# Performance work log

Measured on AMD Instinct MI355X. Metric: run time of the kernel, lower is better.

The kernel has to match this reference:

```python
import jax, jax.numpy as jnp
import numpy as np
import math

V, D, H, NL, ML = 30000, 1024, 16, 6, 1024
B, L = 2, 1024
DH = D // H
HID = D // 2  # BoundaryLayer hidden_dim = d_model // 2


def _ln(x, g, b):
    # torch LayerNorm: biased variance, eps=1e-5
    m = x.mean(-1, keepdims=True)
    v = jnp.var(x, axis=-1, keepdims=True)
    return (x - m) * jax.lax.rsqrt(v + 1e-5) * g + b


def setup_inputs() -> dict:
    key = jax.random.key(0)
    ks = iter(jax.random.split(key, 64))
    nrm = lambda shape, std=0.02: jax.random.normal(next(ks), shape, jnp.float32) * std

    def xav(shape):
        # xavier_uniform over last two dims (fan_in, fan_out) per layer
        fan_in, fan_out = shape[-2], shape[-1]
        bound = math.sqrt(6.0 / (fan_in + fan_out))
        return jax.random.uniform(next(ks), shape, jnp.float32, -bound, bound)

    inp = {
        "ids": jax.random.randint(next(ks), (B, L), 0, V),
        "embed": nrm((V, D)),              # tied with head
        "pos_enc": nrm((1, ML, D)),
        # per-layer stacked params
        "rg_w": nrm((NL, D, 4)),
        "rg_b": jnp.zeros((NL, 4)),
        "qkv_w": xav((NL, D, 3 * D)),
        "qkv_b": jnp.zeros((NL, 3 * D)),
        "out_w": xav((NL, D, D)),
        "out_b": jnp.zeros((NL, D)),
        "ph_w": xav((NL, D, H)),
        "ph_b": jnp.zeros((NL, H)),
        "res_scale": jnp.full((NL,), 0.1, jnp.float32),
        "ph_scale": jnp.ones((NL,), jnp.float32),
        "ff1_w": xav((NL, D, 4 * D)),
        "ff1_b": jnp.zeros((NL, 4 * D)),
        "ff2_w": xav((NL, 4 * D, D)),
        "ff2_b": jnp.zeros((NL, D)),
        "n1_g": jnp.ones((NL, D)),
        "n1_b": jnp.zeros((NL, D)),
        "n2_g": jnp.ones((NL, D)),
        "n2_b": jnp.zeros((NL, D)),
        # shared boundary MLP
        "bnd_w1": xav((D, HID)),
        "bnd_b1": jnp.zeros((HID,)),
        "bnd_w2": xav((HID, 1)),
        "bnd_b2": jnp.zeros((1,)),
        "fn_g": jnp.ones((D,)),
        "fn_b": jnp.zeros((D,)),
    }
    return inp


def reference(ids, embed, pos_enc, rg_w, rg_b, qkv_w, qkv_b, out_w, out_b,
              ph_w, ph_b, res_scale, ph_scale, ff1_w, ff1_b, ff2_w, ff2_b,
              n1_g, n1_b, n2_g, n2_b, bnd_w1, bnd_b1, bnd_w2, bnd_b2, fn_g, fn_b):
    b, l = ids.shape
    d = embed.shape[1]
    nl = rg_w.shape[0]
    h = ph_w.shape[-1]
    dh = d // h

    x = embed[ids] * math.sqrt(d) + pos_enc[:, :l, :]
    grammar, shocks = [], []
    for i in range(nl):
        # R-Grammar modulation
        rg = jax.nn.sigmoid(x @ rg_w[i] + rg_b[i])                  # [B,L,4]
        grammar.append(rg)
        xm = x * (1.0 + 0.1 * rg.mean(-1, keepdims=True))
        # resonance attention (pre-norm)
        a_in = _ln(xm, n1_g[i], n1_b[i])
        qkv = (a_in @ qkv_w[i] + qkv_b[i]).reshape(b, l, 3, h, dh)
        qkv = jnp.transpose(qkv, (2, 0, 3, 1, 4))                   # [3,B,H,L,dh]
        q, k, v = qkv[0], qkv[1], qkv[2]
        scores = jnp.einsum('bhld,bhmd->bhlm', q, k) / math.sqrt(dh)
        pv = jnp.tanh(ph_scale[i] * (a_in @ ph_w[i] + ph_b[i]))     # [B,L,H]
        pv = jnp.transpose(pv, (0, 2, 1))                           # [B,H,L]
        phase_diff = (pv[..., :, None] - pv[..., None, :]) ** 2     # [B,H,L,L]
        scores = scores - res_scale[i] * phase_diff
        aw = jax.nn.softmax(scores, axis=-1)
        o = jnp.einsum('bhlm,bhmd->bhld', aw, v)
        o = jnp.transpose(o, (0, 2, 1, 3)).reshape(b, l, d)
        x = xm + (o @ out_w[i] + out_b[i])
        # feed-forward (exact GELU, matching torch default)
        f_in = _ln(x, n2_g[i], n2_b[i])
        ff = jax.nn.gelu(f_in @ ff1_w[i] + ff1_b[i], approximate=False) @ ff2_w[i] + ff2_b[i]
        x = x + ff
        # boundary shock score (shared MLP)
        shock = jax.nn.sigmoid(jnp.tanh(x @ bnd_w1 + bnd_b1) @ bnd_w2 + bnd_b2)  # [B,L,1]
        shocks.append(shock)
    x = _ln(x, fn_g, fn_b)
    logits = x @ embed.T                                            # tied head
    gs = jnp.stack(grammar, 0)   # [NL,B,L,4]
    ss = jnp.stack(shocks, 0)    # [NL,B,L,1]
    return (logits, x, gs.mean(0), ss.mean(0), gs, ss)
```

## Files before the change

kernel.cpp:

```cpp
#include <hip/hip_runtime.h>
#include <math.h>

constexpr int NLAYER = 6;
constexpr int B_ = 2;
constexpr int L_ = 1024;
constexpr int D_ = 1024;
constexpr int H_ = 16;
constexpr int DH_ = 64;
constexpr int V_ = 30000;
constexpr int HID_ = 512;
constexpr int BL_ = B_ * L_;

typedef __bf16 bf16_t;
typedef bf16_t bf16x8 __attribute__((ext_vector_type(8)));
typedef bf16_t bf16x4 __attribute__((ext_vector_type(4)));
typedef float  f32x4  __attribute__((ext_vector_type(4)));

#define GLOAD_LDS16(gp, lp)                                                    \
    __builtin_amdgcn_global_load_lds(                                          \
        (const __attribute__((address_space(1))) void*)(gp),                   \
        (__attribute__((address_space(3))) void*)(lp), 16, 0, 0)

__device__ __forceinline__ float sigmoidf_(float z) { return 1.0f / (1.0f + __expf(-z)); }
__device__ __forceinline__ float tanhf_(float z) {
    float a = fabsf(z);
    float e = __expf(-2.0f * a);
    float r = (1.0f - e) / (1.0f + e);
    return copysignf(r, z);
}
__device__ __forceinline__ float gelu_exact_(float z) {
    return 0.5f * z * (1.0f + erff(z * 0.70710678118654752440f));
}

__device__ __forceinline__ bf16x8 pack8_(const float* __restrict__ src) {
    float4 f0 = *(const float4*)(src);
    float4 f1 = *(const float4*)(src + 4);
    bf16x8 v;
    v[0] = (bf16_t)f0.x; v[1] = (bf16_t)f0.y; v[2] = (bf16_t)f0.z; v[3] = (bf16_t)f0.w;
    v[4] = (bf16_t)f1.x; v[5] = (bf16_t)f1.y; v[6] = (bf16_t)f1.z; v[7] = (bf16_t)f1.w;
    return v;
}

__device__ __forceinline__ float block_sum_(float v, float* red) {
    int tid = threadIdx.x;
    red[tid] = v; __syncthreads();
    #pragma unroll
    for (int s = 128; s > 0; s >>= 1) {
        if (tid < s) red[tid] += red[tid + s];
        __syncthreads();
    }
    float r = red[0];
    __syncthreads();
    return r;
}

__global__ __launch_bounds__(256) void embed_k(
    const int* __restrict__ ids, const float* __restrict__ emb,
    const float* __restrict__ pos, float* __restrict__ x)
{
    int t = blockIdx.x, tid = threadIdx.x;
    int id = ids[t];
    int l = t % L_;
    #pragma unroll
    for (int it = 0; it < 4; ++it) {
        int d = it * 256 + tid;
        x[(size_t)t * D_ + d] = emb[(size_t)id * D_ + d] * 32.0f + pos[(size_t)l * D_ + d];
    }
}

__global__ __launch_bounds__(256) void tcw_k(
    const float* s0, bf16_t* d0, int K0, int N0, int c0,
    const float* s1, bf16_t* d1, int K1, int N1, int c1,
    const float* s2, bf16_t* d2, int K2, int N2, int c2,
    const float* s3, bf16_t* d3, int K3, int N3, int c3)
{
    __shared__ float t32[32][33];
    int bid = blockIdx.x;
    const float* s; bf16_t* d; int K, N, base;
    if (bid < c0)      { s = s0; d = d0; K = K0; N = N0; base = 0; }
    else if (bid < c1) { s = s1; d = d1; K = K1; N = N1; base = c0; }
    else if (bid < c2) { s = s2; d = d2; K = K2; N = N2; base = c1; }
    else               { s = s3; d = d3; K = K3; N = N3; base = c2; }
    int tt = bid - base;
    int KT = K >> 5;
    int kt = tt % KT, nt = tt / KT;
    int tid = threadIdx.x, cx = tid & 31, ry = tid >> 5;
    #pragma unroll
    for (int j = 0; j < 4; ++j)
        t32[ry + 8 * j][cx] = s[(size_t)(kt * 32 + ry + 8 * j) * N + nt * 32 + cx];
    __syncthreads();
    int r = tid >> 3, c4 = (tid & 7) * 4;
    bf16x4 v;
    #pragma unroll
    for (int j = 0; j < 4; ++j) v[j] = (bf16_t)t32[c4 + j][r];
    *(bf16x4*)(d + (size_t)(nt * 32 + r) * K + kt * 32 + c4) = v;
}

__global__ __launch_bounds__(256) void cvtb_k(
    const float* __restrict__ s, bf16_t* __restrict__ d, int n8)
{
    for (int i = blockIdx.x * 256 + threadIdx.x; i < n8; i += gridDim.x * 256)
        *(bf16x8*)(d + (size_t)i * 8) = pack8_(s + (size_t)i * 8);
}

__global__ __launch_bounds__(256) void rg_xm_ln_k(
    const float* __restrict__ x, const float* __restrict__ rgw,
    const float* __restrict__ rgb, const float* __restrict__ g,
    const float* __restrict__ b, const float* __restrict__ phw,
    const float* __restrict__ phb, const float* __restrict__ ps_p,
    float* __restrict__ xm, bf16_t* __restrict__ ainb,
    float* __restrict__ pvb, float* __restrict__ gs_out)
{
    int t = blockIdx.x, tid = threadIdx.x;
    __shared__ float xr[D_];
    __shared__ float red[256];
    __shared__ float rgsh[4];

    #pragma unroll
    for (int it = 0; it < 4; ++it) {
        int d = it * 256 + tid;
        xr[d] = x[(size_t)t * D_ + d];
    }
    __syncthreads();

    float a0 = 0.f, a1 = 0.f, a2 = 0.f, a3 = 0.f;
    #pragma unroll
    for (int it = 0; it < 4; ++it) {
        int d = it * 256 + tid;
        float xv = xr[d];
        float4 w = *(const float4*)(rgw + (size_t)d * 4);
        a0 += xv * w.x; a1 += xv * w.y; a2 += xv * w.z; a3 += xv * w.w;
    }
    float s0 = block_sum_(a0, red);
    float s1 = block_sum_(a1, red);
    float s2 = block_sum_(a2, red);
    float s3 = block_sum_(a3, red);
    if (tid == 0) {
        float r0 = sigmoidf_(s0 + rgb[0]);
        float r1 = sigmoidf_(s1 + rgb[1]);
        float r2 = sigmoidf_(s2 + rgb[2]);
        float r3 = sigmoidf_(s3 + rgb[3]);
        rgsh[0] = r0; rgsh[1] = r1; rgsh[2] = r2; rgsh[3] = r3;
        gs_out[(size_t)t * 4 + 0] = r0;
        gs_out[(size_t)t * 4 + 1] = r1;
        gs_out[(size_t)t * 4 + 2] = r2;
        gs_out[(size_t)t * 4 + 3] = r3;
    }
    __syncthreads();
    float factor = 1.0f + 0.025f * (rgsh[0] + rgsh[1] + rgsh[2] + rgsh[3]);

    float sm = 0.f, sq = 0.f;
    float vals[4];
    #pragma unroll
    for (int it = 0; it < 4; ++it) {
        int d = it * 256 + tid;
        float v = xr[d] * factor;
        vals[it] = v;
        xm[(size_t)t * D_ + d] = v;
        sm += v; sq += v * v;
    }
    float mean = block_sum_(sm, red) * (1.0f / D_);
    float msq  = block_sum_(sq, red) * (1.0f / D_);
    float rstd = rsqrtf(msq - mean * mean + 1e-5f);
    #pragma unroll
    for (int it = 0; it < 4; ++it) {
        int d = it * 256 + tid;
        float a = (vals[it] - mean) * rstd * g[d] + b[d];
        ainb[(size_t)t * D_ + d] = (bf16_t)a;
        xr[d] = a;
    }
    __syncthreads();

    {
        int c = tid & 15, grp = tid >> 4;
        float acc = 0.f;
        int k0 = grp * 64;
        #pragma unroll
        for (int kk = 0; kk < 64; ++kk)
            acc += xr[k0 + kk] * phw[(size_t)(k0 + kk) * H_ + c];
        red[tid] = acc;
        __syncthreads();
        if (tid < 16) {
            float s = 0.f;
            #pragma unroll
            for (int gg = 0; gg < 16; ++gg) s += red[gg * 16 + tid];
            pvb[(size_t)t * H_ + tid] = tanhf_(ps_p[0] * (s + phb[tid]));
        }
    }
}

__global__ __launch_bounds__(256) void ln_k(
    const float* __restrict__ in, const float* __restrict__ g,
    const float* __restrict__ b, float* __restrict__ outp,
    bf16_t* __restrict__ outb)
{
    int t = blockIdx.x, tid = threadIdx.x;
    __shared__ float red[256];
    float s1 = 0.f, s2 = 0.f;
    float vals[4];
    #pragma unroll
    for (int it = 0; it < 4; ++it) {
        int d = it * 256 + tid;
        float v = in[(size_t)t * D_ + d];
        vals[it] = v; s1 += v; s2 += v * v;
    }
    float mean = block_sum_(s1, red) * (1.0f / D_);
    float msq  = block_sum_(s2, red) * (1.0f / D_);
    float rstd = rsqrtf(msq - mean * mean + 1e-5f);
    #pragma unroll
    for (int it = 0; it < 4; ++it) {
        int d = it * 256 + tid;
        float v = (vals[it] - mean) * rstd * g[d] + b[d];
        if (outp) outp[(size_t)t * D_ + d] = v;
        if (outb) outb[(size_t)t * D_ + d] = (bf16_t)v;
    }
}

template<int BN>
__global__ __launch_bounds__(256) void gemm_bf_k(
    const bf16_t* __restrict__ A, const bf16_t* __restrict__ Bm,
    const float* __restrict__ bias, const float* __restrict__ resid,
    float* __restrict__ C, bf16_t* __restrict__ Cb,
    int M, int N, int K, int MT, int GW,
    int act, const float* __restrict__ scale_ptr)
{
    constexpr int BM = 128;
    constexpr int BK = 64;
    constexpr int WN = BN / 32;

    __shared__ alignas(16) bf16_t As[BM][BK];
    __shared__ alignas(16) bf16_t Bs[BN][BK];

    const int tid  = threadIdx.x;
    const int lane = tid & 63;
    const int w    = tid >> 6;

    int per = MT * GW;
    int grp = blockIdx.x / per;
    int r   = blockIdx.x % per;
    int mi  = r % MT;
    int ni  = grp * GW + r / MT;
    const int bm = mi * BM;
    const int bn = ni * BN;

    const int wr = (w & 1) * 64;
    const int wc = (w >> 1) * (BN / 2);
    const int rlo = lane & 15, lhi = lane >> 4;
    const int srow = lane >> 3;
    const int scol = (lane & 7) * 8;

    f32x4 acc[4][WN];
    #pragma unroll
    for (int m = 0; m < 4; ++m)
        #pragma unroll
        for (int n = 0; n < WN; ++n) {
            f32x4 z = {0.f, 0.f, 0.f, 0.f};
            acc[m][n] = z;
        }

    for (int kt = 0; kt < K; kt += BK) {
        __syncthreads();
        #pragma unroll
        for (int i = 0; i < 4; ++i) {
            int is = w * 4 + i;
            const bf16_t* gp = A + (size_t)(bm + is * 8 + srow) * K + kt + scol;
            GLOAD_LDS16(gp, &As[is * 8][0]);
        }
        #pragma unroll
        for (int i = 0; i < BN / 32; ++i) {
            int is = w * (BN / 32) + i;
            int row = bn + is * 8 + srow;
            if (row > N - 1) row = N - 1;
            const bf16_t* gp = Bm + (size_t)row * K + kt + scol;
            GLOAD_LDS16(gp, &Bs[is * 8][0]);
        }
        __syncthreads();

        #pragma unroll
        for (int h2 = 0; h2 < 2; ++h2) {
            int ko = h2 * 32 + lhi * 8;
            bf16x8 af[4], bfr[WN];
            #pragma unroll
            for (int m = 0; m < 4; ++m)
                af[m] = *(const bf16x8*)(&As[wr + m * 16 + rlo][ko]);
            #pragma unroll
            for (int n = 0; n < WN; ++n)
                bfr[n] = *(const bf16x8*)(&Bs[wc + n * 16 + rlo][ko]);
            #pragma unroll
            for (int m = 0; m < 4; ++m)
                #pragma unroll
                for (int n = 0; n < WN; ++n)
                    acc[m][n] = __builtin_amdgcn_mfma_f32_16x16x32_bf16(
                        af[m], bfr[n], acc[m][n], 0, 0, 0);
        }
    }

    float scale = scale_ptr ? scale_ptr[0] : 1.0f;
    #pragma unroll
    for (int m = 0; m < 4; ++m) {
        #pragma unroll
        for (int n = 0; n < WN; ++n) {
            int col = bn + wc + n * 16 + rlo;
            if (col >= N) continue;
            #pragma unroll
            for (int i = 0; i < 4; ++i) {
                int row = bm + wr + m * 16 + lhi * 4 + i;
                float v = acc[m][n][i];
                if (bias) v += bias[col];
                if (act == 1)      v = gelu_exact_(v);
                else if (act == 2) v = tanhf_(scale * v);
                if (resid) v += resid[(size_t)row * N + col];
                if (C)  C[(size_t)row * N + col] = v;
                if (Cb) Cb[(size_t)row * N + col] = (bf16_t)v;
            }
        }
    }
}

__global__ __launch_bounds__(256) void attn_mfma_k(
    const bf16_t* __restrict__ qkv, const float* __restrict__ pv,
    const float* __restrict__ res_scale_p, bf16_t* __restrict__ o)
{
    constexpr int QB = 64;
    constexpr int NB = 64;

    __shared__ alignas(16) bf16_t Ks[NB][DH_];
    __shared__ alignas(16) bf16_t Vt[DH_][NB];
    __shared__ alignas(16) bf16_t Pl[4][16][NB];
    __shared__ float pvq_s[QB];
    __shared__ float pvk_s[NB];

    const int qt = blockIdx.x, h = blockIdx.y, b = blockIdx.z;
    const int tid = threadIdx.x;
    const int lane = tid & 63, w = tid >> 6;
    const int rlo = lane & 15, lhi = lane >> 4, l7 = lane & 7;
    const float rs = res_scale_p[0];

    const size_t rowbase = (size_t)(b * L_ + qt * QB);

    bf16x8 qf[2];
    {
        const bf16_t* qrow = qkv + (rowbase + w * 16 + rlo) * 3072 + h * DH_;
        #pragma unroll
        for (int kk = 0; kk < 2; ++kk)
            qf[kk] = *(const bf16x8*)(qrow + kk * 32 + lhi * 8);
    }
    if (tid < QB) pvq_s[tid] = pv[(rowbase + tid) * H_ + h];
    __syncthreads();
    float pvq_r[4];
    #pragma unroll
    for (int r = 0; r < 4; ++r) pvq_r[r] = pvq_s[w * 16 + lhi * 4 + r];

    float m_r[4], l_r[4];
    f32x4 acc_o[4];
    #pragma unroll
    for (int r = 0; r < 4; ++r) { m_r[r] = -1e30f; l_r[r] = 0.f; }
    #pragma unroll
    for (int n = 0; n < 4; ++n) {
        f32x4 z = {0.f, 0.f, 0.f, 0.f};
        acc_o[n] = z;
    }

    bf16_t* pw = &Pl[w][0][0];

    for (int k0 = 0; k0 < L_; k0 += NB) {
        __syncthreads();
        #pragma unroll
        for (int i = 0; i < 2; ++i) {
            int sid = i * 256 + tid;
            int row = sid >> 3, s = sid & 7;
            bf16x8 v = *(const bf16x8*)(qkv + (size_t)(b * L_ + k0 + row) * 3072
                                        + 1024 + h * DH_ + s * 8);
            *(bf16x8*)(&Ks[row][(s ^ (row & 7)) * 8]) = v;
        }
        {
            int col4 = (tid & 15) * 4;
            int kb   = tid >> 4;
            bf16x4 rv[4];
            #pragma unroll
            for (int j = 0; j < 4; ++j)
                rv[j] = *(const bf16x4*)(qkv + (size_t)(b * L_ + k0 + kb * 4 + j) * 3072
                                         + 2048 + h * DH_ + col4);
            #pragma unroll
            for (int jj = 0; jj < 4; ++jj) {
                int col = col4 + jj;
                bf16x4 v;
                #pragma unroll
                for (int j = 0; j < 4; ++j)
                    v[j] = rv[j][jj];
                *(bf16x4*)(&Vt[col][((kb >> 1) ^ (col & 7)) * 8 + (kb & 1) * 4]) = v;
            }
        }
        if (tid < NB) pvk_s[tid] = pv[(size_t)(b * L_ + k0 + tid) * H_ + h];
        __syncthreads();

        f32x4 sacc[4];
        #pragma unroll
        for (int n = 0; n < 4; ++n) {
            f32x4 z = {0.f, 0.f, 0.f, 0.f};
            sacc[n] = z;
        }
        __builtin_amdgcn_s_setprio(1);
        #pragma unroll
        for (int kk = 0; kk < 2; ++kk) {
            int soff = ((kk * 4 + lhi) ^ l7) * 8;
            bf16x8 kf[4];
            #pragma unroll
            for (int n = 0; n < 4; ++n)
                kf[n] = *(const bf16x8*)(&Ks[n * 16 + rlo][soff]);
            #pragma unroll
            for (int n = 0; n < 4; ++n)
                sacc[n] = __builtin_amdgcn_mfma_f32_16x16x32_bf16(
                    qf[kk], kf[n], sacc[n], 0, 0, 0);
        }
        __builtin_amdgcn_s_setprio(0);

        float sv[4][4];
        float tmax[4] = {-1e30f, -1e30f, -1e30f, -1e30f};
        #pragma unroll
        for (int n = 0; n < 4; ++n) {
            float pvk = pvk_s[n * 16 + rlo];
            #pragma unroll
            for (int r = 0; r < 4; ++r) {
                float dd = pvq_r[r] - pvk;
                float s = sacc[n][r] * 0.125f - rs * dd * dd;
                sv[n][r] = s;
                tmax[r] = fmaxf(tmax[r], s);
            }
        }
        #pragma unroll
        for (int st = 1; st < 16; st <<= 1)
            #pragma unroll
            for (int r = 0; r < 4; ++r)
                tmax[r] = fmaxf(tmax[r], __shfl_xor(tmax[r], st));

        float tsum[4] = {0.f, 0.f, 0.f, 0.f};
        #pragma unroll
        for (int r = 0; r < 4; ++r) {
            float mn = fmaxf(m_r[r], tmax[r]);
            float sc = __expf(m_r[r] - mn);
            m_r[r] = mn;
            l_r[r] *= sc;
            #pragma unroll
            for (int n = 0; n < 4; ++n) acc_o[n][r] *= sc;
        }
        #pragma unroll
        for (int n = 0; n < 4; ++n) {
            int key = n * 16 + rlo;
            #pragma unroll
            for (int r = 0; r < 4; ++r) {
                float p = __expf(sv[n][r] - m_r[r]);
                tsum[r] += p;
                int q = lhi * 4 + r;
                pw[q * NB + (((key >> 3) ^ (q & 7)) * 8 + (key & 7))] = (bf16_t)p;
            }
        }
        #pragma unroll
        for (int st = 1; st < 16; st <<= 1)
            #pragma unroll
            for (int r = 0; r < 4; ++r)
                tsum[r] += __shfl_xor(tsum[r], st);
        #pragma unroll
        for (int r = 0; r < 4; ++r) l_r[r] += tsum[r];

        __builtin_amdgcn_s_setprio(1);
        #pragma unroll
        for (int kk = 0; kk < 2; ++kk) {
            int soff = ((kk * 4 + lhi) ^ l7) * 8;
            bf16x8 pa = *(const bf16x8*)(pw + rlo * NB + (((kk * 4 + lhi) ^ (rlo & 7)) * 8));
            bf16x8 vf[4];
            #pragma unroll
            for (int n = 0; n < 4; ++n)
                vf[n] = *(const bf16x8*)(&Vt[n * 16 + rlo][soff]);
            #pragma unroll
            for (int n = 0; n < 4; ++n)
                acc_o[n] = __builtin_amdgcn_mfma_f32_16x16x32_bf16(
                    pa, vf[n], acc_o[n], 0, 0, 0);
        }
        __builtin_amdgcn_s_setprio(0);
    }

    float inv[4];
    #pragma unroll
    for (int r = 0; r < 4; ++r) inv[r] = 1.0f / l_r[r];
    #pragma unroll
    for (int n = 0; n < 4; ++n)
        #pragma unroll
        for (int r = 0; r < 4; ++r)
            o[(rowbase + w * 16 + lhi * 4 + r) * D_ + h * DH_ + n * 16 + rlo] =
                (bf16_t)(acc_o[n][r] * inv[r]);
}

__global__ __launch_bounds__(256) void bnd2_k(
    const float* __restrict__ hbuf, const float* __restrict__ w2,
    const float* __restrict__ b2, float* __restrict__ ss_out)
{
    int t = blockIdx.x, tid = threadIdx.x;
    __shared__ float red[256];
    float acc = 0.f;
    #pragma unroll
    for (int it = 0; it < 2; ++it) {
        int d = it * 256 + tid;
        acc += hbuf[(size_t)t * HID_ + d] * w2[d];
    }
    float s = block_sum_(acc, red);
    if (tid == 0) ss_out[t] = sigmoidf_(s + b2[0]);
}

__global__ __launch_bounds__(256) void means_k(
    const float* __restrict__ gs, const float* __restrict__ ss,
    float* __restrict__ gsm, float* __restrict__ ssm)
{
    int i = blockIdx.x * 256 + threadIdx.x;
    if (i < BL_ * 4) {
        float s = 0.f;
        #pragma unroll
        for (int l = 0; l < NLAYER; ++l) s += gs[(size_t)l * BL_ * 4 + i];
        gsm[i] = s * (1.0f / NLAYER);
    }
    if (i < BL_) {
        float s = 0.f;
        #pragma unroll
        for (int l = 0; l < NLAYER; ++l) s += ss[(size_t)l * BL_ + i];
        ssm[i] = s * (1.0f / NLAYER);
    }
}

extern "C" void kernel_launch(void* const* d_in, const int* in_sizes, int n_in,
                              void* d_out, int out_size, void* d_ws, size_t ws_size,
                              hipStream_t stream) {
    const int*   ids       = (const int*)  d_in[0];
    const float* embed     = (const float*)d_in[1];
    const float* pos_enc   = (const float*)d_in[2];
    const float* rg_w      = (const float*)d_in[3];
    const float* rg_b      = (const float*)d_in[4];
    const float* qkv_w     = (const float*)d_in[5];
    const float* qkv_b     = (const float*)d_in[6];
    const float* out_w     = (const float*)d_in[7];
    const float* out_b     = (const float*)d_in[8];
    const float* ph_w      = (const float*)d_in[9];
    const float* ph_b      = (const float*)d_in[10];
    const float* res_scale = (const float*)d_in[11];
    const float* ph_scale  = (const float*)d_in[12];
    const float* ff1_w     = (const float*)d_in[13];
    const float* ff1_b     = (const float*)d_in[14];
    const float* ff2_w     = (const float*)d_in[15];
    const float* ff2_b     = (const float*)d_in[16];
    const float* n1_g      = (const float*)d_in[17];
    const float* n1_b      = (const float*)d_in[18];
    const float* n2_g      = (const float*)d_in[19];
    const float* n2_b      = (const float*)d_in[20];
    const float* bnd_w1    = (const float*)d_in[21];
    const float* bnd_b1    = (const float*)d_in[22];
    const float* bnd_w2    = (const float*)d_in[23];
    const float* bnd_b2    = (const float*)d_in[24];
    const float* fn_g      = (const float*)d_in[25];
    const float* fn_b      = (const float*)d_in[26];

    float* out = (float*)d_out;
    float* ws  = (float*)d_ws;

    const size_t M1 = 1024 * 1024;
    float*  x    = ws;
    float*  xm   = ws + 2 * M1;
    float*  bndh = ws + 4 * M1;
    float*  pvb  = ws + 5 * M1;
    bf16_t* ainb = (bf16_t*)(ws + 5 * M1 + M1 / 4);
    bf16_t* aob  = (bf16_t*)(ws + 6 * M1 + M1 / 4);
    bf16_t* xb   = (bf16_t*)(ws + 7 * M1 + M1 / 4);
    bf16_t* qkvb = (bf16_t*)(ws + 8 * M1 + M1 / 4);
    bf16_t* ffhb = (bf16_t*)(ws + 11 * M1 + M1 / 4);
    float*  wT   = ws + 15 * M1 + M1 / 4;
    bf16_t* qkvT = (bf16_t*)(wT);
    bf16_t* outT = (bf16_t*)(wT + 1572864);
    bf16_t* ff1T = (bf16_t*)(wT + 2097152);
    bf16_t* ff2T = (bf16_t*)(wT + 4194304);
    bf16_t* bndT = (bf16_t*)(wT + 6291456);
    bf16_t* embB = qkvb;

    const size_t o_logits = 0;
    const size_t o_x      = (size_t)BL_ * V_;
    const size_t o_gsm    = o_x + (size_t)BL_ * D_;
    const size_t o_ssm    = o_gsm + (size_t)BL_ * 4;
    const size_t o_gs     = o_ssm + (size_t)BL_;
    const size_t o_ss     = o_gs + (size_t)NLAYER * BL_ * 4;

    embed_k<<<BL_, 256, 0, stream>>>(ids, embed, pos_enc, x);

    tcw_k<<<512, 256, 0, stream>>>(
        bnd_w1, bndT, D_, HID_, 512,
        bnd_w1, bndT, D_, HID_, 512,
        bnd_w1, bndT, D_, HID_, 512,
        bnd_w1, bndT, D_, HID_, 512);

    const int MT = BL_ / 128;

    for (int i = 0; i < NLAYER; ++i) {
        tcw_k<<<12288, 256, 0, stream>>>(
            qkv_w + (size_t)i * D_ * 3 * D_,    qkvT, D_,     3 * D_, 3072,
            out_w + (size_t)i * D_ * D_,        outT, D_,     D_,     4096,
            ff1_w + (size_t)i * D_ * 4 * D_,    ff1T, D_,     4 * D_, 8192,
            ff2_w + (size_t)i * 4 * D_ * D_,    ff2T, 4 * D_, D_,     12288);

        rg_xm_ln_k<<<BL_, 256, 0, stream>>>(
            x, rg_w + (size_t)i * D_ * 4, rg_b + (size_t)i * 4,
            n1_g + (size_t)i * D_, n1_b + (size_t)i * D_,
            ph_w + (size_t)i * D_ * H_, ph_b + (size_t)i * H_, ph_scale + i,
            xm, ainb, pvb, out + o_gs + (size_t)i * BL_ * 4);

        gemm_bf_k<128><<<MT * 24, 256, 0, stream>>>(
            ainb, qkvT, qkv_b + (size_t)i * 3 * D_, nullptr,
            nullptr, qkvb, BL_, 3 * D_, D_, MT, 4, 0, nullptr);

        dim3 ga(L_ / 64, H_, B_);
        attn_mfma_k<<<ga, 256, 0, stream>>>(qkvb, pvb, res_scale + i, aob);

        gemm_bf_k<64><<<MT * 16, 256, 0, stream>>>(
            aob, outT, out_b + (size_t)i * D_, xm,
            x, nullptr, BL_, D_, D_, MT, 4, 0, nullptr);

        ln_k<<<BL_, 256, 0, stream>>>(x, n2_g + (size_t)i * D_, n2_b + (size_t)i * D_,
                                      nullptr, ainb);

        gemm_bf_k<128><<<MT * 32, 256, 0, stream>>>(
            ainb, ff1T, ff1_b + (size_t)i * 4 * D_, nullptr,
            nullptr, ffhb, BL_, 4 * D_, D_, MT, 4, 1, nullptr);

        gemm_bf_k<64><<<MT * 16, 256, 0, stream>>>(
            ffhb, ff2T, ff2_b + (size_t)i * D_, x,
            x, xb, BL_, D_, 4 * D_, MT, 4, 0, nullptr);

        gemm_bf_k<64><<<MT * 8, 256, 0, stream>>>(
            xb, bndT, bnd_b1, nullptr,
            bndh, nullptr, BL_, HID_, D_, MT, 4, 2, nullptr);

        bnd2_k<<<BL_, 256, 0, stream>>>(bndh, bnd_w2, bnd_b2, out + o_ss + (size_t)i * BL_);
    }

    ln_k<<<BL_, 256, 0, stream>>>(x, fn_g, fn_b, out + o_x, xb);

    cvtb_k<<<4096, 256, 0, stream>>>(embed, embB, V_ * D_ / 8);

    gemm_bf_k<128><<<MT * 235, 256, 0, stream>>>(
        xb, embB, nullptr, nullptr,
        out + o_logits, nullptr, BL_, V_, D_, MT, 5, 0, nullptr);

    means_k<<<(BL_ * 4 + 255) / 256, 256, 0, stream>>>(
        out + o_gs, out + o_ss, out + o_gsm, out + o_ssm);
}
```

Baseline: 2.587 ms.

## Double-buffer attention K/V tiles via registers and XOR-swizzle GEMM LDS tiles

The attention kernel now prefetches the next K/V/phase tile into registers while computing on the current tile, then writes it to a second LDS buffer. This halves the barriers per iteration and hides global load latency behind the MFMA work. Separately, the GEMM's A/B LDS tiles get an XOR swizzle on the 16-byte column segment to reduce bank conflicts on fragment reads. The cost is extra LDS for the double buffers and extra registers held live across the loop.

```diff
diff --git a/kernel.cpp b/kernel.cpp
--- a/kernel.cpp
+++ b/kernel.cpp
@@ -247,7 +247,8 @@
     const int wc = (w >> 1) * (BN / 2);
     const int rlo = lane & 15, lhi = lane >> 4;
     const int srow = lane >> 3;
-    const int scol = (lane & 7) * 8;
+    const int scol = ((lane & 7) ^ srow) * 8;
+    const int rsw  = rlo & 7;
 
     f32x4 acc[4][WN];
     #pragma unroll
@@ -278,7 +279,7 @@
 
         #pragma unroll
         for (int h2 = 0; h2 < 2; ++h2) {
-            int ko = h2 * 32 + lhi * 8;
+            int ko = ((h2 * 4 + lhi) ^ rsw) * 8;
             bf16x8 af[4], bfr[WN];
             #pragma unroll
             for (int m = 0; m < 4; ++m)
@@ -323,12 +324,13 @@
 {
     constexpr int QB = 64;
     constexpr int NB = 64;
-
-    __shared__ alignas(16) bf16_t Ks[NB][DH_];
-    __shared__ alignas(16) bf16_t Vt[DH_][NB];
+    constexpr int NT = L_ / NB;
+
+    __shared__ alignas(16) bf16_t Ks[2][NB][DH_];
+    __shared__ alignas(16) bf16_t Vt[2][DH_][NB];
     __shared__ alignas(16) bf16_t Pl[4][16][NB];
     __shared__ float pvq_s[QB];
-    __shared__ float pvk_s[NB];
+    __shared__ float pvk_s[2][NB];
 
     const int qt = blockIdx.x, h = blockIdx.y, b = blockIdx.z;
     const int tid = threadIdx.x;
@@ -338,6 +340,10 @@
 
     const size_t rowbase = (size_t)(b * L_ + qt * QB);
 
+    const int krow0 = tid >> 3,  kseg0 = tid & 7;
+    const int krow1 = krow0 + 32;
+    const int vcol4 = (tid & 15) * 4, vkb = tid >> 4;
+
     bf16x8 qf[2];
     {
         const bf16_t* qrow = qkv + (rowbase + w * 16 + rlo) * 3072 + h * DH_;
@@ -346,6 +352,42 @@
             qf[kk] = *(const bf16x8*)(qrow + kk * 32 + lhi * 8);
     }
     if (tid < QB) pvq_s[tid] = pv[(rowbase + tid) * H_ + h];
+
+    bf16x8 kreg0, kreg1;
+    bf16x4 vreg[4];
+    float pvkr = 0.f;
+
+    #define STAGE_LOAD(k0)                                                         \
+    {                                                                              \
+        kreg0 = *(const bf16x8*)(qkv + (size_t)(b * L_ + (k0) + krow0) * 3072      \
+                                 + 1024 + h * DH_ + kseg0 * 8);                    \
+        kreg1 = *(const bf16x8*)(qkv + (size_t)(b * L_ + (k0) + krow1) * 3072      \
+                                 + 1024 + h * DH_ + kseg0 * 8);                    \
+        _Pragma("unroll")                                                          \
+        for (int j = 0; j < 4; ++j)                                                \
+            vreg[j] = *(const bf16x4*)(qkv + (size_t)(b * L_ + (k0) + vkb * 4 + j) \
+                                       * 3072 + 2048 + h * DH_ + vcol4);           \
+        if (tid < NB) pvkr = pv[(size_t)(b * L_ + (k0) + tid) * H_ + h];           \
+    }
+
+    #define STAGE_WRITE(bf)                                                        \
+    {                                                                              \
+        *(bf16x8*)(&Ks[bf][krow0][(kseg0 ^ (krow0 & 7)) * 8]) = kreg0;             \
+        *(bf16x8*)(&Ks[bf][krow1][(kseg0 ^ (krow1 & 7)) * 8]) = kreg1;             \
+        _Pragma("unroll")                                                          \
+        for (int jj = 0; jj < 4; ++jj) {                                           \
+            int col = vcol4 + jj;                                                  \
+            bf16x4 vv;                                                             \
+            _Pragma("unroll")                                                      \
+            for (int j = 0; j < 4; ++j) vv[j] = vreg[j][jj];                       \
+            *(bf16x4*)(&Vt[bf][col][((vkb >> 1) ^ (col & 7)) * 8 + (vkb & 1) * 4]) \
+                = vv;                                                              \
+        }                                                                          \
+        if (tid < NB) pvk_s[bf][tid] = pvkr;                                       \
+    }
+
+    STAGE_LOAD(0);
+    STAGE_WRITE(0);
     __syncthreads();
     float pvq_r[4];
     #pragma unroll
@@ -363,36 +405,9 @@
 
     bf16_t* pw = &Pl[w][0][0];
 
-    for (int k0 = 0; k0 < L_; k0 += NB) {
-        __syncthreads();
-        #pragma unroll
-        for (int i = 0; i < 2; ++i) {
-            int sid = i * 256 + tid;
-            int row = sid >> 3, s = sid & 7;
-            bf16x8 v = *(const bf16x8*)(qkv + (size_t)(b * L_ + k0 + row) * 3072
-                                        + 1024 + h * DH_ + s * 8);
-            *(bf16x8*)(&Ks[row][(s ^ (row & 7)) * 8]) = v;
-        }
-        {
-            int col4 = (tid & 15) * 4;
-            int kb   = tid >> 4;
-            bf16x4 rv[4];
-            #pragma unroll
-            for (int j = 0; j < 4; ++j)
-                rv[j] = *(const bf16x4*)(qkv + (size_t)(b * L_ + k0 + kb * 4 + j) * 3072
-                                         + 2048 + h * DH_ + col4);
-            #pragma unroll
-            for (int jj = 0; jj < 4; ++jj) {
-                int col = col4 + jj;
-                bf16x4 v;
-                #pragma unroll
-                for (int j = 0; j < 4; ++j)
-                    v[j] = rv[j][jj];
-                *(bf16x4*)(&Vt[col][((kb >> 1) ^ (col & 7)) * 8 + (kb & 1) * 4]) = v;
-            }
-        }
-        if (tid < NB) pvk_s[tid] = pv[(size_t)(b * L_ + k0 + tid) * H_ + h];
-        __syncthreads();
+    for (int t = 0; t < NT; ++t) {
+        const int cur = t & 1;
+        if (t + 1 < NT) STAGE_LOAD((t + 1) * NB);
 
         f32x4 sacc[4];
         #pragma unroll
@@ -407,7 +422,7 @@
             bf16x8 kf[4];
             #pragma unroll
             for (int n = 0; n < 4; ++n)
-                kf[n] = *(const bf16x8*)(&Ks[n * 16 + rlo][soff]);
+                kf[n] = *(const bf16x8*)(&Ks[cur][n * 16 + rlo][soff]);
             #pragma unroll
             for (int n = 0; n < 4; ++n)
                 sacc[n] = __builtin_amdgcn_mfma_f32_16x16x32_bf16(
@@ -419,7 +434,7 @@
         float tmax[4] = {-1e30f, -1e30f, -1e30f, -1e30f};
         #pragma unroll
         for (int n = 0; n < 4; ++n) {
-            float pvk = pvk_s[n * 16 + rlo];
+            float pvk = pvk_s[cur][n * 16 + rlo];
             #pragma unroll
             for (int r = 0; r < 4; ++r) {
                 float dd = pvq_r[r] - pvk;
@@ -471,13 +486,18 @@
             bf16x8 vf[4];
             #pragma unroll
             for (int n = 0; n < 4; ++n)
-                vf[n] = *(const bf16x8*)(&Vt[n * 16 + rlo][soff]);
+                vf[n] = *(const bf16x8*)(&Vt[cur][n * 16 + rlo][soff]);
             #pragma unroll
             for (int n = 0; n < 4; ++n)
                 acc_o[n] = __builtin_amdgcn_mfma_f32_16x16x32_bf16(
                     pa, vf[n], acc_o[n], 0, 0, 0);
         }
         __builtin_amdgcn_s_setprio(0);
+
+        if (t + 1 < NT) {
+            STAGE_WRITE(cur ^ 1);
+            __syncthreads();
+        }
     }
 
     float inv[4];
@@ -489,6 +509,9 @@
         for (int r = 0; r < 4; ++r)
             o[(rowbase + w * 16 + lhi * 4 + r) * D_ + h * DH_ + n * 16 + rlo] =
                 (bf16_t)(acc_o[n][r] * inv[r]);
+
+    #undef STAGE_LOAD
+    #undef STAGE_WRITE
 }
 
 __global__ __launch_bounds__(256) void bnd2_k(
```

Result: faster. 2.485 ms (-4.0%).
